# Performance work log

Measured on AMD Instinct MI355X. Metric: run time of the kernel, lower is better.

Reference implementation:

```python
import jax, jax.numpy as jnp
import numpy as np

B, NQ, NKV, K = 2, 1024, 2048, 64
D, H, LAT = 1024, 16, 128
HD = D // H
SCALE = 1.0 / np.sqrt(HD)


def setup_inputs() -> dict:
    key = jax.random.key(0)
    ks = jax.random.split(key, 7)
    s = lambda fan_in: 1.0 / np.sqrt(fan_in)
    return {
        "x_q": jax.random.normal(ks[0], (B, NQ, D), jnp.float32),
        "x_kv": jax.random.normal(ks[1], (B, NKV, D), jnp.float32),
        "indices": jax.random.randint(ks[2], (B, NQ, K), 0, NKV),
        "W_q": jax.random.normal(ks[3], (D, D), jnp.float32) * s(D),
        "W_kv_down": jax.random.normal(ks[4], (LAT, D), jnp.float32) * s(D),
        "W_kv_up": jax.random.normal(ks[5], (2 * D, LAT), jnp.float32) * s(LAT),
        "W_out": jax.random.normal(ks[6], (D, D), jnp.float32) * s(D),
    }


def reference(x_q, x_kv, indices, W_q, W_kv_down, W_kv_up, W_out):
    b, nq, d = x_q.shape
    # q: (B, NQ, H, HD)
    q = (x_q @ W_q.T).reshape(b, nq, H, HD)
    # latent KV cache: (B, NKV, LAT)
    c_kv = x_kv @ W_kv_down.T
    # per-query gather of selected latents: (B, NQ, K, LAT)
    c_sel = c_kv[jnp.arange(b)[:, None, None], indices]
    # up-project to k/v heads: (B, NQ, K, 2, H, HD)
    kv = (c_sel @ W_kv_up.T).reshape(b, nq, K, 2, H, HD)
    k = kv[:, :, :, 0]  # (B, NQ, K, H, HD)
    v = kv[:, :, :, 1]
    # selective attention: scores over the K selected positions
    scores = jnp.einsum("bqhd,bqkhd->bqkh", q, k) * SCALE
    attn = jax.nn.softmax(scores, axis=2)
    out = jnp.einsum("bqkh,bqkhd->bqhd", attn, v).reshape(b, nq, d)
    return out @ W_out.T
```

## Files before the change

### kernel.cpp

```cpp
#include <hip/hip_runtime.h>

#define NKVc  2048
#define SCALE 0.125f

typedef unsigned short u16;
typedef __attribute__((ext_vector_type(8))) short short8b;
typedef __attribute__((ext_vector_type(8))) unsigned short ushort8;
typedef __attribute__((ext_vector_type(4))) float f32x4;

__device__ __forceinline__ u16 f2bf(float f) {
  unsigned int u = __float_as_uint(f);
  return (u16)((u + 0x7FFFu + ((u >> 16) & 1u)) >> 16);
}

__device__ __forceinline__ void conv8(const float* __restrict__ in,
                                      u16* __restrict__ out, int j) {
  float4 f0 = ((const float4*)in)[j * 2];
  float4 f1 = ((const float4*)in)[j * 2 + 1];
  ushort4 a, b;
  a.x = f2bf(f0.x); a.y = f2bf(f0.y); a.z = f2bf(f0.z); a.w = f2bf(f0.w);
  b.x = f2bf(f1.x); b.y = f2bf(f1.y); b.z = f2bf(f1.z); b.w = f2bf(f1.w);
  ((ushort4*)out)[j * 2] = a;
  ((ushort4*)out)[j * 2 + 1] = b;
}

__global__ __launch_bounds__(256)
void megaconv(const float* __restrict__ xq, const float* __restrict__ wq,
              const float* __restrict__ xkv, const float* __restrict__ wkvd,
              const float* __restrict__ wkvu, const float* __restrict__ wout,
              u16* __restrict__ xq_bf, u16* __restrict__ wq_bf,
              u16* __restrict__ xkv_bf, u16* __restrict__ wkvd_bf,
              u16* __restrict__ wv_bf, u16* __restrict__ wout_bf,
              u16* __restrict__ wkt) {
  int i = blockIdx.x * 256 + threadIdx.x;
  if (i < 262144) { conv8(xq, xq_bf, i); return; }
  if (i < 393216) { conv8(wq, wq_bf, i - 262144); return; }
  if (i < 917504) { conv8(xkv, xkv_bf, i - 393216); return; }
  if (i < 933888) { conv8(wkvd, wkvd_bf, i - 917504); return; }
  if (i < 950272) { conv8(wkvu + 131072, wv_bf, i - 933888); return; }
  if (i < 1081344) { conv8(wout, wout_bf, i - 950272); return; }
  {
    int o = (i - 1081344) * 8;
    int hd0 = o & 63;
    int l = (o >> 6) & 127;
    int h = o >> 13;
    const float* src = wkvu + (h * 64 + hd0) * 128 + l;
    ushort8 v;
#pragma unroll
    for (int j = 0; j < 8; ++j) v[j] = f2bf(src[j * 128]);
    *(ushort8*)&wkt[o] = v;
  }
}

template<int NSUB>
__device__ __forceinline__ void gemm_body(
    int bx, int by, int bz,
    const u16* __restrict__ A, int lda, long sAz,
    const u16* __restrict__ B, int ldb, long sBz,
    float* __restrict__ C, u16* __restrict__ Cb,
    int ldc, long sCz, int K, bool obf) {
  A += (size_t)bz * sAz;
  B += (size_t)bz * sBz;
  __shared__ __align__(16) u16 As[2][NSUB * 256 * 8];
  __shared__ __align__(16) u16 Bs[2][NSUB * 256 * 8];
  const int tid = threadIdx.x;
  const int w = tid >> 6, lane = tid & 63;
  const int bm = by * 64, bn = bx * 64;
  const int wr = w >> 1, wc = w & 1;

  f32x4 acc[2][2] = {};

  auto stage = [&](int buf, int t) {
#pragma unroll
    for (int sub = 0; sub < NSUB; ++sub) {
      int s = w * 64 + lane;
      int row = s >> 2;
      int kc = (s & 3) ^ ((row >> 1) & 3);
      int kg = t * (NSUB * 32) + sub * 32 + kc * 8;
      {
        const u16* g = A + (size_t)(bm + row) * lda + kg;
        __builtin_amdgcn_global_load_lds(
            (const __attribute__((address_space(1))) unsigned int*)g,
            (__attribute__((address_space(3))) unsigned int*)&As[buf][(sub * 256 + w * 64) * 8],
            16, 0, 0);
      }
      {
        const u16* g = B + (size_t)(bn + row) * ldb + kg;
        __builtin_amdgcn_global_load_lds(
            (const __attribute__((address_space(1))) unsigned int*)g,
            (__attribute__((address_space(3))) unsigned int*)&Bs[buf][(sub * 256 + w * 64) * 8],
            16, 0, 0);
      }
    }
  };

  auto compute = [&](int buf) {
#pragma unroll
    for (int sub = 0; sub < NSUB; ++sub) {
      short8b a[2], b[2];
#pragma unroll
      for (int m = 0; m < 2; ++m) {
        int row = wr * 32 + m * 16 + (lane & 15);
        int slot = sub * 256 + row * 4 + ((lane >> 4) ^ ((row >> 1) & 3));
        a[m] = *(const short8b*)&As[buf][slot * 8];
      }
#pragma unroll
      for (int n = 0; n < 2; ++n) {
        int col = wc * 32 + n * 16 + (lane & 15);
        int slot = sub * 256 + col * 4 + ((lane >> 4) ^ ((col >> 1) & 3));
        b[n] = *(const short8b*)&Bs[buf][slot * 8];
      }
#pragma unroll
      for (int m = 0; m < 2; ++m)
#pragma unroll
        for (int n = 0; n < 2; ++n)
          acc[m][n] = __builtin_amdgcn_mfma_f32_16x16x32_bf16(a[m], b[n], acc[m][n], 0, 0, 0);
    }
  };

  stage(0, 0);
  asm volatile("s_waitcnt vmcnt(0)" ::: "memory");
  __syncthreads();
  const int nk = K / (NSUB * 32);
  for (int t = 0; t < nk; ++t) {
    int cur = t & 1;
    if (t + 1 < nk) stage(cur ^ 1, t + 1);
    compute(cur);
    asm volatile("s_waitcnt vmcnt(0)" ::: "memory");
    __syncthreads();
  }

#pragma unroll
  for (int m = 0; m < 2; ++m) {
    int row0 = bm + wr * 32 + m * 16 + (lane >> 4) * 4;
#pragma unroll
    for (int n = 0; n < 2; ++n) {
      int col = bn + wc * 32 + n * 16 + (lane & 15);
      if (obf) {
        u16* Cz = Cb + (size_t)bz * sCz;
#pragma unroll
        for (int r = 0; r < 4; ++r)
          Cz[(size_t)(row0 + r) * ldc + col] = f2bf(acc[m][n][r]);
      } else {
        float* Cz = C + (size_t)bz * sCz;
#pragma unroll
        for (int r = 0; r < 4; ++r)
          Cz[(size_t)(row0 + r) * ldc + col] = acc[m][n][r];
      }
    }
  }
}

__global__ __launch_bounds__(256)
void gemm_nt_g4(const u16* __restrict__ A, int lda, long sAz,
                const u16* __restrict__ B, int ldb, long sBz,
                float* __restrict__ C, u16* __restrict__ Cb,
                int ldc, long sCz, int K, int obf) {
  gemm_body<4>(blockIdx.x, blockIdx.y, blockIdx.z, A, lda, sAz, B, ldb, sBz,
               C, Cb, ldc, sCz, K, obf != 0);
}

__global__ __launch_bounds__(256)
void d1_qproj_ckv(const u16* __restrict__ xq_bf, const u16* __restrict__ wq_bf,
                  const u16* __restrict__ xkv_bf, const u16* __restrict__ wkvd_bf,
                  u16* __restrict__ q_bf, u16* __restrict__ c_kvb) {
  int b = blockIdx.x;
  if (b < 512) {
    gemm_body<2>(b & 15, b >> 4, 0, xq_bf, 1024, 0, wq_bf, 1024, 0,
                 nullptr, q_bf, 1024, 0, 1024, true);
  } else {
    int b2 = b - 512;
    gemm_body<2>(b2 & 1, b2 >> 1, 0, xkv_bf, 1024, 0, wkvd_bf, 1024, 0,
                 nullptr, c_kvb, 128, 0, 1024, true);
  }
}

__global__ __launch_bounds__(256)
void d2_qlat(const u16* __restrict__ q_bf, const u16* __restrict__ wkt,
             u16* __restrict__ qlat_bf) {
  int b = blockIdx.x;
  int bz = b >> 6, r = b & 63;
  gemm_body<2>(r & 1, r >> 1, bz, q_bf, 1024, 64, wkt, 64, 8192,
               nullptr, qlat_bf, 2048, 128, 64, true);
}

__global__ __launch_bounds__(256)
void attn_mfma(const u16* __restrict__ c_kvb,
               const u16* __restrict__ q_latb,
               const int* __restrict__ indices,
               u16* __restrict__ cw_bf) {
  __shared__ __align__(16) u16 qls[256 * 8];
  __shared__ __align__(16) u16 csa[1024 * 8];
  __shared__ __align__(16) u16 cst[128 * 72];
  __shared__ __align__(16) u16 pT[16 * 72];
  __shared__ __align__(16) float redmax[64];
  __shared__ __align__(16) float redsum[64];
  __shared__ __align__(16) u16 outst[2048];

  const int tid = threadIdx.x;
  const int w = tid >> 6, lane = tid & 63;
  const int bq = blockIdx.x;
  const int b = bq >> 10;

  {
    int h = tid >> 4, c = tid & 15;
    ushort8 v = *(const ushort8*)(q_latb + (size_t)bq * 2048 + tid * 8);
    *(ushort8*)&qls[(h * 16 + (c ^ h)) * 8] = v;
  }
  {
    int kidx = indices[bq * 64 + lane];
    const u16* src = c_kvb + ((size_t)b * NKVc + kidx) * 128 + w * 32;
    ushort8 v[4];
#pragma unroll
    for (int t = 0; t < 4; ++t) v[t] = *(const ushort8*)(src + t * 8);
#pragma unroll
    for (int t = 0; t < 4; ++t) {
      int c = w * 4 + t;
      *(ushort8*)&csa[(lane * 16 + (c ^ (lane & 15))) * 8] = v[t];
    }
#pragma unroll
    for (int t = 0; t < 4; ++t)
#pragma unroll
      for (int j = 0; j < 8; ++j)
        cst[(w * 32 + t * 8 + j) * 72 + lane] = v[t][j];
  }
  __syncthreads();

  f32x4 sacc = {};
#pragma unroll
  for (int kc = 0; kc < 4; ++kc) {
    int ar = w * 16 + (lane & 15);
    int ac = kc * 4 + (lane >> 4);
    short8b av = *(const short8b*)&csa[(ar * 16 + (ac ^ (ar & 15))) * 8];
    int bh = lane & 15;
    short8b bv = *(const short8b*)&qls[(bh * 16 + (ac ^ bh)) * 8];
    sacc = __builtin_amdgcn_mfma_f32_16x16x32_bf16(av, bv, sacc, 0, 0, 0);
  }
  float s0 = sacc[0] * SCALE, s1 = sacc[1] * SCALE;
  float s2 = sacc[2] * SCALE, s3 = sacc[3] * SCALE;
  float mx = fmaxf(fmaxf(s0, s1), fmaxf(s2, s3));
  mx = fmaxf(mx, __shfl_xor(mx, 16));
  mx = fmaxf(mx, __shfl_xor(mx, 32));
  if (lane < 16) redmax[w * 16 + lane] = mx;
  __syncthreads();
  const int h = lane & 15;
  float m4 = fmaxf(fmaxf(redmax[h], redmax[16 + h]),
                   fmaxf(redmax[32 + h], redmax[48 + h]));
  float p0 = __expf(s0 - m4), p1 = __expf(s1 - m4);
  float p2 = __expf(s2 - m4), p3 = __expf(s3 - m4);
  float sm = p0 + p1 + p2 + p3;
  sm += __shfl_xor(sm, 16);
  sm += __shfl_xor(sm, 32);
  if (lane < 16) redsum[w * 16 + lane] = sm;
  __syncthreads();
  float tot = redsum[h] + redsum[16 + h] + redsum[32 + h] + redsum[48 + h];
  float inv = 1.0f / tot;
  {
    ushort4 pw;
    pw.x = f2bf(p0 * inv); pw.y = f2bf(p1 * inv);
    pw.z = f2bf(p2 * inv); pw.w = f2bf(p3 * inv);
    *(ushort4*)&pT[h * 72 + w * 16 + (lane >> 4) * 4] = pw;
  }
  __syncthreads();

  f32x4 pacc0 = {}, pacc1 = {};
#pragma unroll
  for (int kc = 0; kc < 2; ++kc) {
    short8b pa = *(const short8b*)&pT[(lane & 15) * 72 + kc * 32 + (lane >> 4) * 8];
    int cch = kc * 4 + (lane >> 4);
    int n0 = w * 32 + (lane & 15);
    short8b b0 = *(const short8b*)&cst[n0 * 72 + cch * 8];
    short8b b1 = *(const short8b*)&cst[(n0 + 16) * 72 + cch * 8];
    pacc0 = __builtin_amdgcn_mfma_f32_16x16x32_bf16(pa, b0, pacc0, 0, 0, 0);
    pacc1 = __builtin_amdgcn_mfma_f32_16x16x32_bf16(pa, b1, pacc1, 0, 0, 0);
  }
#pragma unroll
  for (int r = 0; r < 4; ++r) {
    int hh = (lane >> 4) * 4 + r;
    outst[hh * 128 + w * 32 + (lane & 15)] = f2bf(pacc0[r]);
    outst[hh * 128 + w * 32 + 16 + (lane & 15)] = f2bf(pacc1[r]);
  }
  __syncthreads();
  *(ushort8*)(cw_bf + (size_t)bq * 2048 + tid * 8) = *(const ushort8*)&outst[tid * 8];
}

extern "C" void kernel_launch(void* const* d_in, const int* in_sizes, int n_in,
                              void* d_out, int out_size, void* d_ws, size_t ws_size,
                              hipStream_t stream) {
  const float* x_q    = (const float*)d_in[0];
  const float* x_kv   = (const float*)d_in[1];
  const int*   idx    = (const int*)  d_in[2];
  const float* W_q    = (const float*)d_in[3];
  const float* W_kvd  = (const float*)d_in[4];
  const float* W_kvu  = (const float*)d_in[5];
  const float* W_out  = (const float*)d_in[6];
  float* out = (float*)d_out;

  char* wsb = (char*)d_ws;
  u16* xq_bf   = (u16*)(wsb + 0);
  u16* wq_bf   = (u16*)(wsb + (4u << 20));
  u16* xkv_bf  = (u16*)(wsb + (6u << 20));
  u16* wkvd_bf = (u16*)(wsb + (14u << 20));
  u16* wkt     = (u16*)(wsb + (14u << 20) + (256u << 10));
  u16* wv_bf   = (u16*)(wsb + (14u << 20) + (512u << 10));
  u16* wout_bf = (u16*)(wsb + (14u << 20) + (768u << 10));
  u16* q_bf    = (u16*)(wsb + (17u << 20));
  u16* c_kvb   = (u16*)(wsb + (21u << 20));
  u16* qlat_bf = (u16*)(wsb + (22u << 20));
  u16* cw_bf   = (u16*)(wsb + (30u << 20));
  u16* o_bf    = (u16*)(wsb + (38u << 20));

  megaconv<<<dim3(4288), 256, 0, stream>>>(x_q, W_q, x_kv, W_kvd, W_kvu, W_out,
                                           xq_bf, wq_bf, xkv_bf, wkvd_bf,
                                           wv_bf, wout_bf, wkt);

  d1_qproj_ckv<<<dim3(640), 256, 0, stream>>>(xq_bf, wq_bf, xkv_bf, wkvd_bf,
                                              q_bf, c_kvb);

  d2_qlat<<<dim3(1024), 256, 0, stream>>>(q_bf, wkt, qlat_bf);

  attn_mfma<<<dim3(2048), 256, 0, stream>>>(c_kvb, qlat_bf, idx, cw_bf);

  gemm_nt_g4<<<dim3(1, 32, 16), 256, 0, stream>>>(
      cw_bf, 2048, 128, wv_bf, 128, 8192, nullptr, o_bf, 1024, 64, 128, 1);

  gemm_nt_g4<<<dim3(16, 32, 1), 256, 0, stream>>>(
      o_bf, 1024, 0, wout_bf, 1024, 0, out, nullptr, 1024, 0, 1024, 0);
}
```

Baseline: 63.69 us.

## Fuse q-projection with per-head latent absorption GEMM in one kernel

The Q projection tile for each head (64 rows × 64 head dims) now stays in LDS as bf16 and is multiplied right away by that head's absorbed W_k^T slice (64×128), producing q_lat directly. This removes the d2_qlat launch and the round trip of q_bf through global memory. The price is a longer per-block tail and some extra LDS traffic on the 512 q blocks. The gemm body is split into loop and epilogue helpers so the fused kernel can reuse them.

```diff
diff --git a/kernel.cpp b/kernel.cpp
--- a/kernel.cpp
+++ b/kernel.cpp
@@ -12,6 +12,11 @@
   unsigned int u = __float_as_uint(f);
   return (u16)((u + 0x7FFFu + ((u >> 16) & 1u)) >> 16);
 }
+
+#define GLOAD16(gp, lp) \
+  __builtin_amdgcn_global_load_lds( \
+      (const __attribute__((address_space(1))) unsigned int*)(gp), \
+      (__attribute__((address_space(3))) unsigned int*)(lp), 16, 0, 0)
 
 __device__ __forceinline__ void conv8(const float* __restrict__ in,
                                       u16* __restrict__ out, int j) {
@@ -53,22 +58,14 @@
 }
 
 template<int NSUB>
-__device__ __forceinline__ void gemm_body(
-    int bx, int by, int bz,
-    const u16* __restrict__ A, int lda, long sAz,
-    const u16* __restrict__ B, int ldb, long sBz,
-    float* __restrict__ C, u16* __restrict__ Cb,
-    int ldc, long sCz, int K, bool obf) {
-  A += (size_t)bz * sAz;
-  B += (size_t)bz * sBz;
-  __shared__ __align__(16) u16 As[2][NSUB * 256 * 8];
-  __shared__ __align__(16) u16 Bs[2][NSUB * 256 * 8];
+__device__ __forceinline__ void gemm_loop(
+    u16* As, u16* Bs, int bm, int bn,
+    const u16* __restrict__ A, int lda,
+    const u16* __restrict__ B, int ldb, int K, f32x4 (&acc)[2][2]) {
   const int tid = threadIdx.x;
   const int w = tid >> 6, lane = tid & 63;
-  const int bm = by * 64, bn = bx * 64;
   const int wr = w >> 1, wc = w & 1;
-
-  f32x4 acc[2][2] = {};
+  constexpr int BUF = NSUB * 256 * 8;
 
   auto stage = [&](int buf, int t) {
 #pragma unroll
@@ -77,20 +74,10 @@
       int row = s >> 2;
       int kc = (s & 3) ^ ((row >> 1) & 3);
       int kg = t * (NSUB * 32) + sub * 32 + kc * 8;
-      {
-        const u16* g = A + (size_t)(bm + row) * lda + kg;
-        __builtin_amdgcn_global_load_lds(
-            (const __attribute__((address_space(1))) unsigned int*)g,
-            (__attribute__((address_space(3))) unsigned int*)&As[buf][(sub * 256 + w * 64) * 8],
-            16, 0, 0);
-      }
-      {
-        const u16* g = B + (size_t)(bn + row) * ldb + kg;
-        __builtin_amdgcn_global_load_lds(
-            (const __attribute__((address_space(1))) unsigned int*)g,
-            (__attribute__((address_space(3))) unsigned int*)&Bs[buf][(sub * 256 + w * 64) * 8],
-            16, 0, 0);
-      }
+      GLOAD16(A + (size_t)(bm + row) * lda + kg,
+              As + buf * BUF + (sub * 256 + w * 64) * 8);
+      GLOAD16(B + (size_t)(bn + row) * ldb + kg,
+              Bs + buf * BUF + (sub * 256 + w * 64) * 8);
     }
   };
 
@@ -102,13 +89,13 @@
       for (int m = 0; m < 2; ++m) {
         int row = wr * 32 + m * 16 + (lane & 15);
         int slot = sub * 256 + row * 4 + ((lane >> 4) ^ ((row >> 1) & 3));
-        a[m] = *(const short8b*)&As[buf][slot * 8];
+        a[m] = *(const short8b*)&As[buf * BUF + slot * 8];
       }
 #pragma unroll
       for (int n = 0; n < 2; ++n) {
         int col = wc * 32 + n * 16 + (lane & 15);
         int slot = sub * 256 + col * 4 + ((lane >> 4) ^ ((col >> 1) & 3));
-        b[n] = *(const short8b*)&Bs[buf][slot * 8];
+        b[n] = *(const short8b*)&Bs[buf * BUF + slot * 8];
       }
 #pragma unroll
       for (int m = 0; m < 2; ++m)
@@ -129,7 +116,14 @@
     asm volatile("s_waitcnt vmcnt(0)" ::: "memory");
     __syncthreads();
   }
-
+}
+
+__device__ __forceinline__ void gemm_epi(
+    f32x4 (&acc)[2][2], int bm, int bn,
+    float* __restrict__ C, u16* __restrict__ Cb, int ldc, bool obf) {
+  const int lane = threadIdx.x & 63;
+  const int w = threadIdx.x >> 6;
+  const int wr = w >> 1, wc = w & 1;
 #pragma unroll
   for (int m = 0; m < 2; ++m) {
     int row0 = bm + wr * 32 + m * 16 + (lane >> 4) * 4;
@@ -137,15 +131,13 @@
     for (int n = 0; n < 2; ++n) {
       int col = bn + wc * 32 + n * 16 + (lane & 15);
       if (obf) {
-        u16* Cz = Cb + (size_t)bz * sCz;
 #pragma unroll
         for (int r = 0; r < 4; ++r)
-          Cz[(size_t)(row0 + r) * ldc + col] = f2bf(acc[m][n][r]);
+          Cb[(size_t)(row0 + r) * ldc + col] = f2bf(acc[m][n][r]);
       } else {
-        float* Cz = C + (size_t)bz * sCz;
 #pragma unroll
         for (int r = 0; r < 4; ++r)
-          Cz[(size_t)(row0 + r) * ldc + col] = acc[m][n][r];
+          C[(size_t)(row0 + r) * ldc + col] = acc[m][n][r];
       }
     }
   }
@@ -156,32 +148,95 @@
                 const u16* __restrict__ B, int ldb, long sBz,
                 float* __restrict__ C, u16* __restrict__ Cb,
                 int ldc, long sCz, int K, int obf) {
-  gemm_body<4>(blockIdx.x, blockIdx.y, blockIdx.z, A, lda, sAz, B, ldb, sBz,
-               C, Cb, ldc, sCz, K, obf != 0);
+  __shared__ __align__(16) u16 As[2 * 1024 * 8];
+  __shared__ __align__(16) u16 Bs[2 * 1024 * 8];
+  f32x4 acc[2][2] = {};
+  gemm_loop<4>(As, Bs, blockIdx.y * 64, blockIdx.x * 64,
+               A + (size_t)blockIdx.z * sAz, lda,
+               B + (size_t)blockIdx.z * sBz, ldb, K, acc);
+  gemm_epi(acc, blockIdx.y * 64, blockIdx.x * 64,
+           C ? C + (size_t)blockIdx.z * sCz : nullptr,
+           Cb ? Cb + (size_t)blockIdx.z * sCz : nullptr, ldc, obf != 0);
 }
 
 __global__ __launch_bounds__(256)
-void d1_qproj_ckv(const u16* __restrict__ xq_bf, const u16* __restrict__ wq_bf,
-                  const u16* __restrict__ xkv_bf, const u16* __restrict__ wkvd_bf,
-                  u16* __restrict__ q_bf, u16* __restrict__ c_kvb) {
-  int b = blockIdx.x;
-  if (b < 512) {
-    gemm_body<2>(b & 15, b >> 4, 0, xq_bf, 1024, 0, wq_bf, 1024, 0,
-                 nullptr, q_bf, 1024, 0, 1024, true);
-  } else {
+void d1_fused(const u16* __restrict__ xq_bf, const u16* __restrict__ wq_bf,
+              const u16* __restrict__ xkv_bf, const u16* __restrict__ wkvd_bf,
+              const u16* __restrict__ wkt, u16* __restrict__ qlat_bf,
+              u16* __restrict__ c_kvb) {
+  __shared__ __align__(16) u16 As[2 * 512 * 8];
+  __shared__ __align__(16) u16 Bs[2 * 512 * 8];
+  const int b = blockIdx.x;
+  const int tid = threadIdx.x;
+  const int w = tid >> 6, lane = tid & 63;
+  const int wr = w >> 1, wc = w & 1;
+  f32x4 acc[2][2] = {};
+
+  if (b >= 512) {
     int b2 = b - 512;
-    gemm_body<2>(b2 & 1, b2 >> 1, 0, xkv_bf, 1024, 0, wkvd_bf, 1024, 0,
-                 nullptr, c_kvb, 128, 0, 1024, true);
-  }
-}
-
-__global__ __launch_bounds__(256)
-void d2_qlat(const u16* __restrict__ q_bf, const u16* __restrict__ wkt,
-             u16* __restrict__ qlat_bf) {
-  int b = blockIdx.x;
-  int bz = b >> 6, r = b & 63;
-  gemm_body<2>(r & 1, r >> 1, bz, q_bf, 1024, 64, wkt, 64, 8192,
-               nullptr, qlat_bf, 2048, 128, 64, true);
+    int bm = (b2 >> 1) * 64, bn = (b2 & 1) * 64;
+    gemm_loop<2>(As, Bs, bm, bn, xkv_bf, 1024, wkvd_bf, 1024, 1024, acc);
+    gemm_epi(acc, bm, bn, nullptr, c_kvb, 128, true);
+    return;
+  }
+
+  const int h = b & 15, bm = (b >> 4) * 64;
+  gemm_loop<2>(As, Bs, bm, h * 64, xq_bf, 1024, wq_bf, 1024, 1024, acc);
+
+#pragma unroll
+  for (int i = 0; i < 4; ++i) {
+    int s = (w * 4 + i) * 64 + lane;
+    int l = s >> 3, c = s & 7;
+    GLOAD16(wkt + h * 8192 + l * 64 + ((c ^ (l & 7)) * 8), Bs + s * 8);
+  }
+#pragma unroll
+  for (int mm = 0; mm < 2; ++mm)
+#pragma unroll
+    for (int nn = 0; nn < 2; ++nn) {
+      int hd = wc * 32 + nn * 16 + (lane & 15);
+      int c = hd >> 3;
+#pragma unroll
+      for (int rr = 0; rr < 4; ++rr) {
+        int row = wr * 32 + mm * 16 + (lane >> 4) * 4 + rr;
+        As[row * 64 + ((c ^ (row & 7)) * 8) + (hd & 7)] = f2bf(acc[mm][nn][rr]);
+      }
+    }
+  asm volatile("s_waitcnt vmcnt(0)" ::: "memory");
+  __syncthreads();
+
+  f32x4 acc2[2][4] = {};
+#pragma unroll
+  for (int ks = 0; ks < 2; ++ks) {
+    short8b af[2], bv[4];
+#pragma unroll
+    for (int mm = 0; mm < 2; ++mm) {
+      int row = wr * 32 + mm * 16 + (lane & 15);
+      int ch = ks * 4 + (lane >> 4);
+      af[mm] = *(const short8b*)&As[row * 64 + ((ch ^ (row & 7)) * 8)];
+    }
+#pragma unroll
+    for (int nf = 0; nf < 4; ++nf) {
+      int l = wc * 64 + nf * 16 + (lane & 15);
+      int ch = ks * 4 + (lane >> 4);
+      bv[nf] = *(const short8b*)&Bs[(l * 8 + (ch ^ (l & 7))) * 8];
+    }
+#pragma unroll
+    for (int mm = 0; mm < 2; ++mm)
+#pragma unroll
+      for (int nf = 0; nf < 4; ++nf)
+        acc2[mm][nf] = __builtin_amdgcn_mfma_f32_16x16x32_bf16(af[mm], bv[nf], acc2[mm][nf], 0, 0, 0);
+  }
+#pragma unroll
+  for (int mm = 0; mm < 2; ++mm) {
+    int row0 = bm + wr * 32 + mm * 16 + (lane >> 4) * 4;
+#pragma unroll
+    for (int nf = 0; nf < 4; ++nf) {
+      int l = wc * 64 + nf * 16 + (lane & 15);
+#pragma unroll
+      for (int r = 0; r < 4; ++r)
+        qlat_bf[(size_t)(row0 + r) * 2048 + h * 128 + l] = f2bf(acc2[mm][nf][r]);
+    }
+  }
 }
 
 __global__ __launch_bounds__(256)
@@ -304,7 +359,6 @@
   u16* wkt     = (u16*)(wsb + (14u << 20) + (256u << 10));
   u16* wv_bf   = (u16*)(wsb + (14u << 20) + (512u << 10));
   u16* wout_bf = (u16*)(wsb + (14u << 20) + (768u << 10));
-  u16* q_bf    = (u16*)(wsb + (17u << 20));
   u16* c_kvb   = (u16*)(wsb + (21u << 20));
   u16* qlat_bf = (u16*)(wsb + (22u << 20));
   u16* cw_bf   = (u16*)(wsb + (30u << 20));
@@ -314,10 +368,8 @@
                                            xq_bf, wq_bf, xkv_bf, wkvd_bf,
                                            wv_bf, wout_bf, wkt);
 
-  d1_qproj_ckv<<<dim3(640), 256, 0, stream>>>(xq_bf, wq_bf, xkv_bf, wkvd_bf,
-                                              q_bf, c_kvb);
-
-  d2_qlat<<<dim3(1024), 256, 0, stream>>>(q_bf, wkt, qlat_bf);
+  d1_fused<<<dim3(640), 256, 0, stream>>>(xq_bf, wq_bf, xkv_bf, wkvd_bf,
+                                          wkt, qlat_bf, c_kvb);
 
   attn_mfma<<<dim3(2048), 256, 0, stream>>>(c_kvb, qlat_bf, idx, cw_bf);
 
```

Measured after the change: 59.24 us. -7.0%, faster.
